# Performance work log

Hardware: AMD Instinct MI355X
Metric: run time of the kernel (lower is better)

Reference implementation:

```python
import jax, jax.numpy as jnp
import numpy as np

B, T, V, E, H = 32, 512, 20000, 300, 512


def setup_inputs() -> dict:
    key = jax.random.key(0)
    k1, k2, k3, k4 = jax.random.split(key, 4)
    tokens = jax.random.randint(k1, (B, T), 0, V, dtype=jnp.int32)
    emb = jax.random.normal(k2, (V, E), dtype=jnp.float32)
    # Keras LSTM: kernel [E, 4H], recurrent_kernel [H, 4H], bias [4H]
    W = jax.random.normal(k3, (E, 4 * H), dtype=jnp.float32) * (1.0 / np.sqrt(E))
    U = jax.random.normal(k4, (H, 4 * H), dtype=jnp.float32) * (1.0 / np.sqrt(H))
    b = jnp.zeros((4 * H,), dtype=jnp.float32)
    return {"tokens": tokens, "emb": emb, "W": W, "U": U, "b": b}


def _lstm_last_state(x, W, U, b):
    # x: [B, T, E].  Gate order (Keras): i, f, g(candidate), o.
    h0 = jnp.zeros((x.shape[0], H), dtype=x.dtype)
    c0 = jnp.zeros((x.shape[0], H), dtype=x.dtype)
    # Precompute input projections for all timesteps: [T, B, 4H]
    xz = jnp.einsum('bte,eg->tbg', x, W) + b

    def step(carry, xz_t):
        h, c = carry
        z = xz_t + h @ U                      # [B, 4H]
        i, f, g, o = jnp.split(z, 4, axis=-1)
        i = jax.nn.sigmoid(i)
        f = jax.nn.sigmoid(f)
        g = jnp.tanh(g)
        o = jax.nn.sigmoid(o)
        c = f * c + i * g
        h = o * jnp.tanh(c)
        return (h, c), None

    (h, c), _ = jax.lax.scan(step, (h0, c0), xz)
    return h, c


def reference(tokens, emb, W, U, b):
    x = emb[tokens]                            # [B, T, E] embedding lookup
    hidden, cell = _lstm_last_state(x, W, U, b)
    return (hidden, cell)                      # Encoder returns (hidden, cell)
```

## Files before the change

### kernel.cpp

```cpp
#include <hip/hip_runtime.h>
#include <hip/hip_bf16.h>

typedef unsigned short u16;
typedef unsigned int u32;
typedef unsigned long long u64;
typedef short  s16x8 __attribute__((ext_vector_type(8)));
typedef float  f32x4 __attribute__((ext_vector_type(4)));
typedef u32    u32x4 __attribute__((ext_vector_type(4)));

#define T_STEPS 512
#define BATCH   32
#define HID     512
#define EMBD    300
#define NGATE   2048

#define XZ_OFF   0ull
#define XZ_BYTES (512ull*32*2048*4)
#define UB_OFF   (XZ_OFF + XZ_BYTES)
#define UB_BYTES (2048ull*512*2)
#define WT_OFF   (UB_OFF + UB_BYTES)
#define WT_BYTES (2048ull*320*2)
#define HB_OFF   (WT_OFF + WT_BYTES)
#define HB_BYTES (2ull*8192*4)
#define CNT_OFF  (HB_OFF + HB_BYTES)
#define CNT_BYTES 1024ull

__device__ inline u16 f2b(float f) {
  u32 u = __builtin_bit_cast(u32, f);
  return (u16)((u + 0x7fffu + ((u >> 16) & 1u)) >> 16);
}

__device__ inline void st32_agent(u32* p, u32 v) {
  __hip_atomic_store(p, v, __ATOMIC_RELAXED, __HIP_MEMORY_SCOPE_AGENT);
}
__device__ inline void st64_agent(u64* p, u64 v) {
  __hip_atomic_store(p, v, __ATOMIC_RELAXED, __HIP_MEMORY_SCOPE_AGENT);
}
__device__ inline u32 ld32_agent(const u32* p) {
  return __hip_atomic_load(p, __ATOMIC_RELAXED, __HIP_MEMORY_SCOPE_AGENT);
}
__device__ inline float ldxz(const float* p) {
  return __builtin_bit_cast(float, ld32_agent((const u32*)p));
}
__device__ inline void wait_pair(const u32* c) {
  int tries = 0;
  while (ld32_agent(c) < 32u) {
    if (++tries > (1 << 22)) break;
    __builtin_amdgcn_s_sleep(2);
  }
}

__global__ __launch_bounds__(64) void pack_w(const float* __restrict__ W, u16* __restrict__ wt) {
  int n = blockIdx.x;
  for (int i = 0; i < 5; ++i) {
    int k = i * 64 + threadIdx.x;
    float v = (k < EMBD) ? W[(size_t)k * NGATE + n] : 0.f;
    u32 off = ((u32)(2 * k)) ^ (((u32)(n & 7)) << 4);
    *(u16*)((char*)wt + (size_t)n * 640 + off) = f2b(v);
  }
}

__global__ __launch_bounds__(64) void pack_u(const float* __restrict__ U, u16* __restrict__ ub) {
  int blk = blockIdx.x;
  int w = blk >> 6, nl = blk & 63;
  int gcol = (nl & 3) * 512 + w * 16 + (nl >> 2);
  for (int i = 0; i < 8; ++i) {
    int k = i * 64 + threadIdx.x;
    float v = U[(size_t)k * NGATE + gcol];
    *(u16*)((char*)ub + (size_t)blk * 1024 + 2 * k) = f2b(v);
  }
}

__global__ __launch_bounds__(256) void fused_enc(const int* __restrict__ tokens,
                                                 const float* __restrict__ emb,
                                                 const u16* __restrict__ wt,
                                                 const float* __restrict__ bias,
                                                 const u16* __restrict__ ub,
                                                 float* __restrict__ xz,
                                                 u32* __restrict__ hbuf,
                                                 u32* __restrict__ cnt,
                                                 float* __restrict__ out) {
  extern __shared__ char smem[];
  const int tid = threadIdx.x;
  const int bid = blockIdx.x;
  const int lane = tid & 63, wv = tid >> 6;

  if (bid >= 32) {
    const int gbid = bid - 32;
    const int mtile = gbid >> 5;
    const int n0 = (gbid & 31) * 64;
    const int t0 = mtile * 2;

    {
      int row = tid >> 2, q = tid & 3;
      int tok = tokens[(row & 31) * 512 + t0 + (row >> 5)];
      const float* er = emb + (size_t)tok * EMBD;
      for (int i = 0; i < 10; ++i) {
        int k = q * 80 + i * 8;
        float4 lo = {0, 0, 0, 0}, hi = {0, 0, 0, 0};
        if (k <= 296) lo = *(const float4*)(er + k);
        if (k <= 292) hi = *(const float4*)(er + k + 4);
        u16 u[8] = {f2b(lo.x), f2b(lo.y), f2b(lo.z), f2b(lo.w),
                    f2b(hi.x), f2b(hi.y), f2b(hi.z), f2b(hi.w)};
        int kc = q * 10 + i;
        *(uint4*)(smem + kc * 1040 + row * 16) = *(uint4*)u;
      }
    }
    {
      const uint4* src = (const uint4*)((const char*)wt + (size_t)n0 * 640);
      for (int i = 0; i < 10; ++i)
        *(uint4*)(smem + 41600 + (i * 256 + tid) * 16) = src[i * 256 + tid];
    }
    __syncthreads();

    const int mq = wv >> 1, nq = wv & 1;
    const int arow = lane & 15, kq4 = lane >> 4;
    f32x4 acc[2][2] = {};
#pragma unroll
    for (int ks = 0; ks < 10; ++ks) {
      s16x8 af[2], bfr[2];
#pragma unroll
      for (int mt = 0; mt < 2; ++mt) {
        int row = mq * 32 + mt * 16 + arow;
        int kc = ks * 4 + kq4;
        af[mt] = *(const s16x8*)(smem + kc * 1040 + row * 16);
      }
#pragma unroll
      for (int nt = 0; nt < 2; ++nt) {
        int nl = nq * 32 + nt * 16 + arow;
        u32 kb = (u32)(ks * 64 + (kq4 << 4));
        bfr[nt] = *(const s16x8*)(smem + 41600 + nl * 640 + (kb ^ (((u32)(nl & 7)) << 4)));
      }
#pragma unroll
      for (int mt = 0; mt < 2; ++mt)
#pragma unroll
        for (int nt = 0; nt < 2; ++nt)
          acc[mt][nt] = __builtin_amdgcn_mfma_f32_16x16x32_bf16(af[mt], bfr[nt], acc[mt][nt], 0, 0, 0);
    }
#pragma unroll
    for (int mt = 0; mt < 2; ++mt)
#pragma unroll
      for (int nt = 0; nt < 2; ++nt) {
        int gn = n0 + nq * 32 + nt * 16 + arow;
        float bv = bias[gn];
        int g = gn >> 9, j = gn & 511;
        size_t inner = (size_t)((j >> 4) * 64 + g * 16 + (j & 15));
#pragma unroll
        for (int r = 0; r < 4; ++r) {
          int lr = mq * 32 + mt * 16 + (kq4 << 2) + r;
          int tt = t0 + (lr >> 5), bb = lr & 31;
          float v = acc[mt][nt][r] + bv;
          st32_agent((u32*)xz + (size_t)(tt * 32 + bb) * 2048 + inner,
                     __builtin_bit_cast(u32, v));
        }
      }
    asm volatile("s_waitcnt vmcnt(0)" ::: "memory");
    __syncthreads();
    if (tid == 0)
      __hip_atomic_fetch_add(&cnt[mtile], 1u, __ATOMIC_RELAXED, __HIP_MEMORY_SCOPE_AGENT);
    return;
  }

  char* hl = smem;
  const int wg = bid;

  const int arow = lane & 15, kq = lane >> 4;
  const int nl = wv * 16 + arow;
  const u32 aswz = ((u32)(arow & 7)) << 4;
  const int j0 = wg * 16;
  const int jl = 4 * wv + kq;
  float c0 = 0.f, c1 = 0.f;

  s16x8 ureg[16];
  {
    const char* up = (const char*)ub + (size_t)(wg * 64 + nl) * 1024 + (kq << 4);
#pragma unroll
    for (int ks = 0; ks < 16; ++ks) ureg[ks] = *(const s16x8*)(up + ks * 64);
  }

  const u32 vo0 = (u32)(tid * 16 + 1 * 4096), vo1 = (u32)(tid * 16 + 3 * 4096);
  const u32 vo2 = (u32)(tid * 16 + 5 * 4096), vo3 = (u32)(tid * 16 + 7 * 4096);
  const u32 hrow0 = (u32)(tid >> 6);
  const u32 hcolb = (u32)((tid & 63) * 16);

  const int pb   = (kq & 1) ? (arow + 16) : arow;
  const u32 pidx64 = (u32)(pb * 128 + wg * 4 + wv);

  float xzv[2][4];
  {
    wait_pair(&cnt[0]);
    const float* p = xz + (size_t)arow * 2048 + wg * 64 + jl;
#pragma unroll
    for (int g = 0; g < 4; ++g) {
      xzv[0][g] = ldxz(p + g * 16);
      xzv[1][g] = ldxz(p + 16 * 2048 + g * 16);
    }
  }
  __syncthreads();

  for (int t = 0; t < T_STEPS; ++t) {
    if (t > 0) {
      u32 tg = (((u32)t >> 1) + 1u) & 3u;
      u32 pat = (tg & 1u) | ((tg >> 1) << 16);
      const u64 sb = (u64)(uintptr_t)hbuf + (u64)((t & 1) * 32768);
      u32x4 q0, q1, q2, q3, q4, q5, q6, q7;
      int tries = 0;
      for (;;) {
        asm volatile(
          "global_load_dwordx4 %0, %8, %12 offset:-4096 sc0 sc1\n\t"
          "global_load_dwordx4 %1, %8, %12 sc0 sc1\n\t"
          "global_load_dwordx4 %2, %9, %12 offset:-4096 sc0 sc1\n\t"
          "global_load_dwordx4 %3, %9, %12 sc0 sc1\n\t"
          "global_load_dwordx4 %4, %10, %12 offset:-4096 sc0 sc1\n\t"
          "global_load_dwordx4 %5, %10, %12 sc0 sc1\n\t"
          "global_load_dwordx4 %6, %11, %12 offset:-4096 sc0 sc1\n\t"
          "global_load_dwordx4 %7, %11, %12 sc0 sc1\n\t"
          "s_waitcnt vmcnt(0)"
          : "=&v"(q0), "=&v"(q1), "=&v"(q2), "=&v"(q3),
            "=&v"(q4), "=&v"(q5), "=&v"(q6), "=&v"(q7)
          : "v"(vo0), "v"(vo1), "v"(vo2), "v"(vo3), "s"(sb)
          : "memory");
        u32 x0 = (q0.x ^ pat) | (q0.y ^ pat) | (q0.z ^ pat) | (q0.w ^ pat);
        u32 x1 = (q1.x ^ pat) | (q1.y ^ pat) | (q1.z ^ pat) | (q1.w ^ pat);
        u32 x2 = (q2.x ^ pat) | (q2.y ^ pat) | (q2.z ^ pat) | (q2.w ^ pat);
        u32 x3 = (q3.x ^ pat) | (q3.y ^ pat) | (q3.z ^ pat) | (q3.w ^ pat);
        u32 x4 = (q4.x ^ pat) | (q4.y ^ pat) | (q4.z ^ pat) | (q4.w ^ pat);
        u32 x5 = (q5.x ^ pat) | (q5.y ^ pat) | (q5.z ^ pat) | (q5.w ^ pat);
        u32 x6 = (q6.x ^ pat) | (q6.y ^ pat) | (q6.z ^ pat) | (q6.w ^ pat);
        u32 x7 = (q7.x ^ pat) | (q7.y ^ pat) | (q7.z ^ pat) | (q7.w ^ pat);
        u32 bad = (x0 | x1 | x2 | x3 | x4 | x5 | x6 | x7) & 0x00010001u;
        if (bad == 0 || ++tries > 65536) break;
        __builtin_amdgcn_s_sleep(1);
      }
#define HW(L, Q) { u32 r_ = hrow0 + 4u * (L);                                  \
        u32 off_ = r_ * 1024u + (hcolb ^ ((r_ & 7u) << 4));                    \
        *(u32x4*)(hl + off_) = (Q); }
      HW(0, q0) HW(1, q1) HW(2, q2) HW(3, q3)
      HW(4, q4) HW(5, q5) HW(6, q6) HW(7, q7)
#undef HW
    }
    __syncthreads();

    f32x4 acc0 = {0, 0, 0, 0}, acc1 = {0, 0, 0, 0};
    if (t > 0) {
#pragma unroll
      for (int ks = 0; ks < 16; ++ks) {
        u32 kb = (u32)(ks * 64 + (kq << 4));
        s16x8 h0 = *(const s16x8*)(hl + arow * 1024 + (kb ^ aswz));
        s16x8 h1 = *(const s16x8*)(hl + (arow + 16) * 1024 + (kb ^ aswz));
        acc0 = __builtin_amdgcn_mfma_f32_16x16x32_bf16(ureg[ks], h0, acc0, 0, 0, 0);
        acc1 = __builtin_amdgcn_mfma_f32_16x16x32_bf16(ureg[ks], h1, acc1, 0, 0, 0);
      }
    }

    float hov[2], cov[2];
#pragma unroll
    for (int e = 0; e < 2; ++e) {
      f32x4 zr = e ? acc1 : acc0;
      float zi = zr[0] + xzv[e][0];
      float zf = zr[1] + xzv[e][1];
      float zg = zr[2] + xzv[e][2];
      float zo = zr[3] + xzv[e][3];
      float ig = 1.f / (1.f + __expf(-zi));
      float fg = 1.f / (1.f + __expf(-zf));
      float gg = 1.f - 2.f / (__expf(2.f * zg) + 1.f);
      float og = 1.f / (1.f + __expf(-zo));
      float cc = e ? c1 : c0;
      cc = fg * cc + ig * gg;
      float hh = og * (1.f - 2.f / (__expf(2.f * cc) + 1.f));
      if (e) c1 = cc; else c0 = cc;
      hov[e] = hh; cov[e] = cc;
    }

    if (t < T_STEPS - 1) {
      u32 pk = (u32)f2b(hov[0]) | ((u32)f2b(hov[1]) << 16);
      u32 pr = (u32)__shfl_xor((int)pk, 16, 64);
      u32 val = (kq & 1) ? ((pr >> 16) | (pk & 0xFFFF0000u))
                         : ((pk & 0xFFFFu) | (pr << 16));
      u32 tg2 = (((u32)(t + 1) >> 1) + 1u) & 3u;
      val = (val & 0xFFFEFFFEu) | (tg2 & 1u) | ((tg2 >> 1) << 16);
      u32 v2 = (u32)__shfl_xor((int)val, 32, 64);
      if (kq < 2) {
        u64 wide = (u64)val | ((u64)v2 << 32);
        st64_agent((u64*)(hbuf + (size_t)((t + 1) & 1) * 8192) + pidx64, wide);
      }
      {
        if (((t + 1) & 1) == 0) wait_pair(&cnt[(t + 1) >> 1]);
        const float* p = xz + ((size_t)(t + 1) * 32 + arow) * 2048 + wg * 64 + jl;
#pragma unroll
        for (int g = 0; g < 4; ++g) {
          xzv[0][g] = ldxz(p + g * 16);
          xzv[1][g] = ldxz(p + 16 * 2048 + g * 16);
        }
      }
    } else {
      int j = j0 + jl;
      out[arow * 512 + j]                 = hov[0];
      out[(arow + 16) * 512 + j]          = hov[1];
      out[16384 + arow * 512 + j]         = cov[0];
      out[16384 + (arow + 16) * 512 + j]  = cov[1];
    }
  }
}

extern "C" void kernel_launch(void* const* d_in, const int* in_sizes, int n_in,
                              void* d_out, int out_size, void* d_ws, size_t ws_size,
                              hipStream_t stream) {
  const int*   tokens = (const int*)d_in[0];
  const float* emb    = (const float*)d_in[1];
  const float* W      = (const float*)d_in[2];
  const float* U      = (const float*)d_in[3];
  const float* bias   = (const float*)d_in[4];
  float* out = (float*)d_out;
  char*  ws  = (char*)d_ws;

  float* xz   = (float*)(ws + XZ_OFF);
  u16*   ub   = (u16*)(ws + UB_OFF);
  u16*   wt   = (u16*)(ws + WT_OFF);
  u32*   hbuf = (u32*)(ws + HB_OFF);
  u32*   cnt  = (u32*)(ws + CNT_OFF);

  hipMemsetAsync(ws + HB_OFF, 0, HB_BYTES + CNT_BYTES, stream);
  pack_w<<<2048, 64, 0, stream>>>(W, wt);
  pack_u<<<2048, 64, 0, stream>>>(U, ub);
  fused_enc<<<32 + 8192, 256, 82560, stream>>>(tokens, emb, wt, bias, ub,
                                               xz, hbuf, cnt, out);
}
```

Before: 1.596 ms.

## Load recurrent h operands directly from global into MFMA registers, skipping LDS staging

Each wave now loads its own copy of the full h state (32 rows by 512) straight from the global exchange buffer into registers laid out as MFMA B operands, replacing the cooperative global-to-LDS copy, the block barrier and the LDS reads. This removes a __syncthreads and the LDS round trip from every recurrent step. In exchange each wave issues four times as many global loads (32 dwordx4 per lane instead of 8 per thread shared across the block), and register pressure rises sharply, hence launch_bounds(256,1).

```diff
diff --git a/kernel.cpp b/kernel.cpp
--- a/kernel.cpp
+++ b/kernel.cpp
@@ -71,15 +71,15 @@
   }
 }
 
-__global__ __launch_bounds__(256) void fused_enc(const int* __restrict__ tokens,
-                                                 const float* __restrict__ emb,
-                                                 const u16* __restrict__ wt,
-                                                 const float* __restrict__ bias,
-                                                 const u16* __restrict__ ub,
-                                                 float* __restrict__ xz,
-                                                 u32* __restrict__ hbuf,
-                                                 u32* __restrict__ cnt,
-                                                 float* __restrict__ out) {
+__global__ __launch_bounds__(256, 1) void fused_enc(const int* __restrict__ tokens,
+                                                    const float* __restrict__ emb,
+                                                    const u16* __restrict__ wt,
+                                                    const float* __restrict__ bias,
+                                                    const u16* __restrict__ ub,
+                                                    float* __restrict__ xz,
+                                                    u32* __restrict__ hbuf,
+                                                    u32* __restrict__ cnt,
+                                                    float* __restrict__ out) {
   extern __shared__ char smem[];
   const int tid = threadIdx.x;
   const int bid = blockIdx.x;
@@ -161,12 +161,9 @@
     return;
   }
 
-  char* hl = smem;
   const int wg = bid;
-
   const int arow = lane & 15, kq = lane >> 4;
   const int nl = wv * 16 + arow;
-  const u32 aswz = ((u32)(arow & 7)) << 4;
   const int j0 = wg * 16;
   const int jl = 4 * wv + kq;
   float c0 = 0.f, c1 = 0.f;
@@ -178,10 +175,8 @@
     for (int ks = 0; ks < 16; ++ks) ureg[ks] = *(const s16x8*)(up + ks * 64);
   }
 
-  const u32 vo0 = (u32)(tid * 16 + 1 * 4096), vo1 = (u32)(tid * 16 + 3 * 4096);
-  const u32 vo2 = (u32)(tid * 16 + 5 * 4096), vo3 = (u32)(tid * 16 + 7 * 4096);
-  const u32 hrow0 = (u32)(tid >> 6);
-  const u32 hcolb = (u32)((tid & 63) * 16);
+  const u32 hvo0 = (u32)(arow * 1024 + kq * 16);
+  const u32 hvo1 = hvo0 + 16384u;
 
   const int pb   = (kq & 1) ? (arow + 16) : arow;
   const u32 pidx64 = (u32)(pb * 128 + wg * 4 + wv);
@@ -196,61 +191,84 @@
       xzv[1][g] = ldxz(p + 16 * 2048 + g * 16);
     }
   }
-  __syncthreads();
 
   for (int t = 0; t < T_STEPS; ++t) {
+    f32x4 acc0 = {0, 0, 0, 0}, acc1 = {0, 0, 0, 0};
     if (t > 0) {
       u32 tg = (((u32)t >> 1) + 1u) & 3u;
       u32 pat = (tg & 1u) | ((tg >> 1) << 16);
       const u64 sb = (u64)(uintptr_t)hbuf + (u64)((t & 1) * 32768);
-      u32x4 q0, q1, q2, q3, q4, q5, q6, q7;
+      u32x4 q0, q1, q2, q3, q4, q5, q6, q7, q8, q9, q10, q11, q12, q13, q14, q15;
+      u32x4 r0, r1, r2, r3, r4, r5, r6, r7, r8, r9, r10, r11, r12, r13, r14, r15;
       int tries = 0;
       for (;;) {
         asm volatile(
-          "global_load_dwordx4 %0, %8, %12 offset:-4096 sc0 sc1\n\t"
-          "global_load_dwordx4 %1, %8, %12 sc0 sc1\n\t"
-          "global_load_dwordx4 %2, %9, %12 offset:-4096 sc0 sc1\n\t"
-          "global_load_dwordx4 %3, %9, %12 sc0 sc1\n\t"
-          "global_load_dwordx4 %4, %10, %12 offset:-4096 sc0 sc1\n\t"
-          "global_load_dwordx4 %5, %10, %12 sc0 sc1\n\t"
-          "global_load_dwordx4 %6, %11, %12 offset:-4096 sc0 sc1\n\t"
-          "global_load_dwordx4 %7, %11, %12 sc0 sc1\n\t"
+          "global_load_dwordx4 %0, %16, %17 sc0 sc1\n\t"
+          "global_load_dwordx4 %1, %16, %17 offset:64 sc0 sc1\n\t"
+          "global_load_dwordx4 %2, %16, %17 offset:128 sc0 sc1\n\t"
+          "global_load_dwordx4 %3, %16, %17 offset:192 sc0 sc1\n\t"
+          "global_load_dwordx4 %4, %16, %17 offset:256 sc0 sc1\n\t"
+          "global_load_dwordx4 %5, %16, %17 offset:320 sc0 sc1\n\t"
+          "global_load_dwordx4 %6, %16, %17 offset:384 sc0 sc1\n\t"
+          "global_load_dwordx4 %7, %16, %17 offset:448 sc0 sc1\n\t"
+          "global_load_dwordx4 %8, %16, %17 offset:512 sc0 sc1\n\t"
+          "global_load_dwordx4 %9, %16, %17 offset:576 sc0 sc1\n\t"
+          "global_load_dwordx4 %10, %16, %17 offset:640 sc0 sc1\n\t"
+          "global_load_dwordx4 %11, %16, %17 offset:704 sc0 sc1\n\t"
+          "global_load_dwordx4 %12, %16, %17 offset:768 sc0 sc1\n\t"
+          "global_load_dwordx4 %13, %16, %17 offset:832 sc0 sc1\n\t"
+          "global_load_dwordx4 %14, %16, %17 offset:896 sc0 sc1\n\t"
+          "global_load_dwordx4 %15, %16, %17 offset:960 sc0 sc1"
+          : "=&v"(q0), "=&v"(q1), "=&v"(q2), "=&v"(q3),
+            "=&v"(q4), "=&v"(q5), "=&v"(q6), "=&v"(q7),
+            "=&v"(q8), "=&v"(q9), "=&v"(q10), "=&v"(q11),
+            "=&v"(q12), "=&v"(q13), "=&v"(q14), "=&v"(q15)
+          : "v"(hvo0), "s"(sb)
+          : "memory");
+        asm volatile(
+          "global_load_dwordx4 %0, %16, %17 sc0 sc1\n\t"
+          "global_load_dwordx4 %1, %16, %17 offset:64 sc0 sc1\n\t"
+          "global_load_dwordx4 %2, %16, %17 offset:128 sc0 sc1\n\t"
+          "global_load_dwordx4 %3, %16, %17 offset:192 sc0 sc1\n\t"
+          "global_load_dwordx4 %4, %16, %17 offset:256 sc0 sc1\n\t"
+          "global_load_dwordx4 %5, %16, %17 offset:320 sc0 sc1\n\t"
+          "global_load_dwordx4 %6, %16, %17 offset:384 sc0 sc1\n\t"
+          "global_load_dwordx4 %7, %16, %17 offset:448 sc0 sc1\n\t"
+          "global_load_dwordx4 %8, %16, %17 offset:512 sc0 sc1\n\t"
+          "global_load_dwordx4 %9, %16, %17 offset:576 sc0 sc1\n\t"
+          "global_load_dwordx4 %10, %16, %17 offset:640 sc0 sc1\n\t"
+          "global_load_dwordx4 %11, %16, %17 offset:704 sc0 sc1\n\t"
+          "global_load_dwordx4 %12, %16, %17 offset:768 sc0 sc1\n\t"
+          "global_load_dwordx4 %13, %16, %17 offset:832 sc0 sc1\n\t"
+          "global_load_dwordx4 %14, %16, %17 offset:896 sc0 sc1\n\t"
+          "global_load_dwordx4 %15, %16, %17 offset:960 sc0 sc1\n\t"
           "s_waitcnt vmcnt(0)"
-          : "=&v"(q0), "=&v"(q1), "=&v"(q2), "=&v"(q3),
-            "=&v"(q4), "=&v"(q5), "=&v"(q6), "=&v"(q7)
-          : "v"(vo0), "v"(vo1), "v"(vo2), "v"(vo3), "s"(sb)
+          : "=&v"(r0), "=&v"(r1), "=&v"(r2), "=&v"(r3),
+            "=&v"(r4), "=&v"(r5), "=&v"(r6), "=&v"(r7),
+            "=&v"(r8), "=&v"(r9), "=&v"(r10), "=&v"(r11),
+            "=&v"(r12), "=&v"(r13), "=&v"(r14), "=&v"(r15)
+          : "v"(hvo1), "s"(sb)
           : "memory");
-        u32 x0 = (q0.x ^ pat) | (q0.y ^ pat) | (q0.z ^ pat) | (q0.w ^ pat);
-        u32 x1 = (q1.x ^ pat) | (q1.y ^ pat) | (q1.z ^ pat) | (q1.w ^ pat);
-        u32 x2 = (q2.x ^ pat) | (q2.y ^ pat) | (q2.z ^ pat) | (q2.w ^ pat);
-        u32 x3 = (q3.x ^ pat) | (q3.y ^ pat) | (q3.z ^ pat) | (q3.w ^ pat);
-        u32 x4 = (q4.x ^ pat) | (q4.y ^ pat) | (q4.z ^ pat) | (q4.w ^ pat);
-        u32 x5 = (q5.x ^ pat) | (q5.y ^ pat) | (q5.z ^ pat) | (q5.w ^ pat);
-        u32 x6 = (q6.x ^ pat) | (q6.y ^ pat) | (q6.z ^ pat) | (q6.w ^ pat);
-        u32 x7 = (q7.x ^ pat) | (q7.y ^ pat) | (q7.z ^ pat) | (q7.w ^ pat);
-        u32 bad = (x0 | x1 | x2 | x3 | x4 | x5 | x6 | x7) & 0x00010001u;
+#define XC(Q) ((Q.x ^ pat) | (Q.y ^ pat) | (Q.z ^ pat) | (Q.w ^ pat))
+        u32 bad = (XC(q0) | XC(q1) | XC(q2) | XC(q3) | XC(q4) | XC(q5) | XC(q6) | XC(q7) |
+                   XC(q8) | XC(q9) | XC(q10) | XC(q11) | XC(q12) | XC(q13) | XC(q14) | XC(q15) |
+                   XC(r0) | XC(r1) | XC(r2) | XC(r3) | XC(r4) | XC(r5) | XC(r6) | XC(r7) |
+                   XC(r8) | XC(r9) | XC(r10) | XC(r11) | XC(r12) | XC(r13) | XC(r14) | XC(r15))
+                  & 0x00010001u;
+#undef XC
         if (bad == 0 || ++tries > 65536) break;
         __builtin_amdgcn_s_sleep(1);
       }
-#define HW(L, Q) { u32 r_ = hrow0 + 4u * (L);                                  \
-        u32 off_ = r_ * 1024u + (hcolb ^ ((r_ & 7u) << 4));                    \
-        *(u32x4*)(hl + off_) = (Q); }
-      HW(0, q0) HW(1, q1) HW(2, q2) HW(3, q3)
-      HW(4, q4) HW(5, q5) HW(6, q6) HW(7, q7)
-#undef HW
-    }
-    __syncthreads();
-
-    f32x4 acc0 = {0, 0, 0, 0}, acc1 = {0, 0, 0, 0};
-    if (t > 0) {
-#pragma unroll
-      for (int ks = 0; ks < 16; ++ks) {
-        u32 kb = (u32)(ks * 64 + (kq << 4));
-        s16x8 h0 = *(const s16x8*)(hl + arow * 1024 + (kb ^ aswz));
-        s16x8 h1 = *(const s16x8*)(hl + (arow + 16) * 1024 + (kb ^ aswz));
-        acc0 = __builtin_amdgcn_mfma_f32_16x16x32_bf16(ureg[ks], h0, acc0, 0, 0, 0);
-        acc1 = __builtin_amdgcn_mfma_f32_16x16x32_bf16(ureg[ks], h1, acc1, 0, 0, 0);
-      }
+#define STEP(KS, Q, R)                                                                   \
+      acc0 = __builtin_amdgcn_mfma_f32_16x16x32_bf16(ureg[KS],                           \
+                 __builtin_bit_cast(s16x8, Q), acc0, 0, 0, 0);                           \
+      acc1 = __builtin_amdgcn_mfma_f32_16x16x32_bf16(ureg[KS],                           \
+                 __builtin_bit_cast(s16x8, R), acc1, 0, 0, 0);
+      STEP(0, q0, r0)   STEP(1, q1, r1)   STEP(2, q2, r2)   STEP(3, q3, r3)
+      STEP(4, q4, r4)   STEP(5, q5, r5)   STEP(6, q6, r6)   STEP(7, q7, r7)
+      STEP(8, q8, r8)   STEP(9, q9, r9)   STEP(10, q10, r10) STEP(11, q11, r11)
+      STEP(12, q12, r12) STEP(13, q13, r13) STEP(14, q14, r14) STEP(15, q15, r15)
+#undef STEP
     }
 
     float hov[2], cov[2];
```

After: 5.746 ms. 260% more time.
